# Performance work log

Measured on AMD Instinct MI355X. Metric: run time of the kernel, lower is better.

Reference implementation:

```python
import jax, jax.numpy as jnp
import numpy as np

N = 10000   # nodes
E = 160000  # edges per layer (avg degree 16)
B = 8       # batch of time windows
CIN = 32
S = 32      # spatial_channels
COUT = 32
NEG_SLOPE = 0.01  # F.leaky_relu default


def _xavier(k, shape):
    bound = np.sqrt(6.0 / (shape[0] + shape[1])).astype(np.float32)
    return jax.random.uniform(k, shape, jnp.float32, -bound, bound)


def setup_inputs() -> dict:
    key = jax.random.key(0)
    ks = jax.random.split(key, 20)
    return {
        "X": jax.random.normal(ks[0], (B, N, CIN), jnp.float32),
        "edge_index0": jax.random.randint(ks[1], (2, E), 0, N, jnp.int32),
        "edge_index1": jax.random.randint(ks[2], (2, E), 0, N, jnp.int32),
        "edge_weight0": jax.random.uniform(ks[3], (E,), jnp.float32),
        "edge_weight1": jax.random.uniform(ks[4], (E,), jnp.float32),
        "res_n_id0": jnp.arange(N, dtype=jnp.int32),
        "res_n_id1": jnp.arange(N, dtype=jnp.int32),
        # layer 1 params
        "Wn1": _xavier(ks[5], (CIN, S)),
        "We1": _xavier(ks[6], (1, S)),
        "Q1": _xavier(ks[7], (S, S)),
        "K1": _xavier(ks[8], (S, S)),
        "att_w1": _xavier(ks[9], (3 * S, 1)),
        "att_b1": jnp.zeros((1,), jnp.float32),
        "out_w1": _xavier(ks[10], (2 * S, S)),
        "out_b1": jnp.zeros((S,), jnp.float32),
        # layer 2 params
        "Wn2": _xavier(ks[11], (S, COUT)),
        "We2": _xavier(ks[12], (1, COUT)),
        "Q2": _xavier(ks[13], (COUT, COUT)),
        "K2": _xavier(ks[14], (COUT, COUT)),
        "att_w2": _xavier(ks[15], (3 * COUT, 1)),
        "att_b2": jnp.zeros((1,), jnp.float32),
        "out_w2": _xavier(ks[16], (2 * COUT, COUT)),
        "out_b2": jnp.zeros((COUT,), jnp.float32),
    }


def _egnn_conv(x_src, x_dst, edge_index, edge_w, Wn, We, Q, K, att_w, att_b, out_w, out_b):
    # x_src: [Ns, B, Cin], x_dst: [Nd, B, Cin], edge_index: [2, E], edge_w: [E]
    xs = x_src @ Wn                              # [Ns, B, O]
    xd = x_dst @ Wn                              # [Nd, B, O]
    ee = edge_w[:, None] @ We                    # [E, O]  (edge_channels = 1)
    src, dst = edge_index[0], edge_index[1]
    xj = xs[src]                                 # [E, B, O] gather source feats
    xi = xd[dst]                                 # [E, B, O] gather target feats
    q = xj @ Q                                   # [E, B, O]
    k = xi @ K                                   # [E, B, O]
    eb = jnp.broadcast_to(ee[:, None, :], q.shape)  # [E, B, O]
    att_feature = jnp.concatenate([q, k, eb], axis=-1)          # [E, B, 3O]
    att = jax.nn.sigmoid(att_feature @ att_w + att_b)           # [E, B, 1]
    msg = att * xj * jax.nn.sigmoid(eb)                         # [E, B, O]
    aggr = jnp.zeros_like(xd).at[dst].add(msg)                  # scatter-add -> [Nd, B, O]
    upd = jnp.concatenate([xd, aggr], axis=-1) @ out_w + out_b  # [Nd, B, O]
    return xd + upd


def reference(X, edge_index0, edge_index1, edge_weight0, edge_weight1,
              res_n_id0, res_n_id1,
              Wn1, We1, Q1, K1, att_w1, att_b1, out_w1, out_b1,
              Wn2, We2, Q2, K2, att_w2, att_b2, out_w2, out_b2):
    h = jnp.transpose(X, (1, 0, 2))              # [N, B, CIN]
    h = _egnn_conv(h, h[res_n_id0], edge_index0, edge_weight0,
                   Wn1, We1, Q1, K1, att_w1, att_b1, out_w1, out_b1)
    h = jax.nn.leaky_relu(h, NEG_SLOPE)
    h = _egnn_conv(h, h[res_n_id1], edge_index1, edge_weight1,
                   Wn2, We2, Q2, K2, att_w2, att_b2, out_w2, out_b2)
    h = jax.nn.leaky_relu(h, NEG_SLOPE)
    return jnp.transpose(h, (1, 0, 2))           # [B, N, COUT]
```

## Files before the change

kernel.cpp:

```cpp
#include <hip/hip_runtime.h>

#define NNODES 10000
#define NEDGES 160000
#define NB 8
#define NC 32
#define CAP 96
#define LUTB 2048
#define EBLKS 625
#define LUTBLKS 128
constexpr float NEG_SLOPE = 0.01f;

__device__ __forceinline__ float sigmoidf_(float x) {
    return 1.0f / (1.0f + __expf(-x));
}

__device__ __forceinline__ unsigned pk2bf(float a, float b) {
    unsigned ua = __float_as_uint(a);
    ua = (ua + 0x7fffu + ((ua >> 16) & 1u)) >> 16;
    unsigned ub = __float_as_uint(b);
    ub = (ub + 0x7fffu + ((ub >> 16) & 1u)) & 0xffff0000u;
    return ua | ub;
}

__global__ __launch_bounds__(256) void prologue_kernel(
    const float* Q1, const float* K1, const float* aw1, const float* We1,
    const float* Q2, const float* K2, const float* aw2, const float* We2,
    const int* __restrict__ ei0, const int* __restrict__ ei1,
    const float* __restrict__ ew0, const float* __restrict__ ew1,
    const float* __restrict__ ab1, const float* __restrict__ ab2,
    float* consts, uint2* __restrict__ lut,
    int2* __restrict__ pkw1, int2* __restrict__ pkw2,
    int* __restrict__ cnt,
    unsigned* __restrict__ xs1h, unsigned* __restrict__ xs2h,
    float* __restrict__ sq1, float* __restrict__ sk1,
    const float* __restrict__ X, const float* __restrict__ Wn)
{
    int bx = blockIdx.x;
    int t = threadIdx.x;

    if (bx < 2 * EBLKS) {
        __shared__ float sCE, sAB;
        int layer = bx / EBLKS;
        int e = (bx % EBLKS) * 256 + t;
        const int*   ei = layer ? ei1 : ei0;
        const float* ew = layer ? ew1 : ew0;
        int src = ei[e];
        int dst = ei[NEDGES + e];
        float w = ew[e];
        if (t < 32) {
            const float* We = layer ? We2 : We1;
            const float* aw = layer ? aw2 : aw1;
            float p = We[t] * aw[64 + t];
            #pragma unroll
            for (int m = 16; m >= 1; m >>= 1) p += __shfl_xor(p, m, 32);
            if (t == 0) { sCE = p; sAB = (layer ? ab2 : ab1)[0]; }
        }
        __syncthreads();
        int pos = atomicAdd(&cnt[layer * NNODES + dst], 1);
        if (pos < CAP) {
            int ix = (int)(w * (float)LUTB);
            ix = min(max(ix, 0), LUTB - 1);
            (layer ? pkw2 : pkw1)[(size_t)dst * CAP + pos] =
                make_int2(src | (ix << 14), __float_as_int(w * sCE + sAB));
        }
        return;
    }
    if (bx < 2 * EBLKS + LUTBLKS) {
        int i = (bx - 2 * EBLKS) * 256 + t;
        int layer = i >> 14;
        int bin   = (i >> 3) & (LUTB - 1);
        int o4    = i & 7;
        float w   = (bin + 0.5f) * (1.0f / LUTB);
        const float* We = layer ? We2 : We1;
        float s0 = sigmoidf_(w * We[o4 * 4 + 0]);
        float s1 = sigmoidf_(w * We[o4 * 4 + 1]);
        float s2 = sigmoidf_(w * We[o4 * 4 + 2]);
        float s3 = sigmoidf_(w * We[o4 * 4 + 3]);
        lut[i] = make_uint2(pk2bf(s0, s1), pk2bf(s2, s3));
        if (i < 128) {
            xs1h[(size_t)NNODES * 128 + i] = 0u;
            xs2h[(size_t)NNODES * 128 + i] = 0u;
        }
        return;
    }
    if (bx == 2 * EBLKS + LUTBLKS) {
        if (t < 32) {
            float aq2 = 0.f, ak2 = 0.f;
            for (int s = 0; s < 32; ++s) {
                aq2 += Q2[t * 32 + s] * aw2[s];
                ak2 += K2[t * 32 + s] * aw2[32 + s];
            }
            consts[64 + t] = aq2;
            consts[96 + t] = ak2;
        }
        return;
    }

    __shared__ float wnL[NC * NC];
    __shared__ float aqL[NC], akL[NC];
    __shared__ float xrow[4][NB][NC + 4];
    int w = t >> 6, l = t & 63, b = l >> 3, o4 = l & 7;
    int n = (bx - (2 * EBLKS + LUTBLKS + 1)) * 4 + w;
    for (int i = t; i < NC * NC; i += 256) wnL[i] = Wn[i];
    if (t < 64) {
        int which = t >> 5, o = t & 31;
        const float* M  = which ? K1 : Q1;
        const float* av = aw1 + which * 32;
        float s = 0.f;
        for (int k = 0; k < 32; ++k) s += M[o * 32 + k] * av[k];
        (which ? akL : aqL)[o] = s;
    }
    const float4* X4 = (const float4*)X;
    float4 xv = X4[((size_t)b * NNODES + n) * 8 + o4];
    ((float4*)&xrow[w][b][0])[o4] = xv;
    __syncthreads();
    float4 aq = ((const float4*)aqL)[o4];
    float4 ak = ((const float4*)akL)[o4];
    const float4* wnL4 = (const float4*)wnL;
    float4 acc = {0.f, 0.f, 0.f, 0.f};
    #pragma unroll
    for (int c = 0; c < NC; ++c) {
        float xc = xrow[w][b][c];
        float4 w4 = wnL4[c * 8 + o4];
        acc.x += xc * w4.x; acc.y += xc * w4.y;
        acc.z += xc * w4.z; acc.w += xc * w4.w;
    }
    ((uint2*)xs1h)[(size_t)n * 64 + l] = make_uint2(pk2bf(acc.x, acc.y), pk2bf(acc.z, acc.w));
    float vq = acc.x * aq.x + acc.y * aq.y + acc.z * aq.z + acc.w * aq.w;
    float vk = acc.x * ak.x + acc.y * ak.y + acc.z * ak.z + acc.w * ak.w;
    #pragma unroll
    for (int m = 4; m >= 1; m >>= 1) {
        vq += __shfl_xor(vq, m);
        vk += __shfl_xor(vk, m);
    }
    if (o4 == 0) {
        sq1[n * NB + b] = vq;
        sk1[n * NB + b] = vk;
    }
}

template <int MODE>
__global__ __launch_bounds__(256) void gather_kernel(
    const int* __restrict__ cnt, const int2* __restrict__ pkw,
    const unsigned* __restrict__ xsh,
    const float* __restrict__ sq, const float* __restrict__ sk,
    const uint2* __restrict__ luth,
    const float* __restrict__ consts,
    const float* __restrict__ ow, const float* __restrict__ ob,
    const float* __restrict__ Wn2,
    unsigned* __restrict__ xs2h, float* __restrict__ sq2, float* __restrict__ sk2,
    float* __restrict__ outp)
{
    __shared__ __align__(16) float owL[2 * NC * NC];
    __shared__ __align__(16) float wnL[(MODE == 0) ? NC * NC : 4];
    __shared__ __align__(16) float xL[4][NB][NC];
    __shared__ __align__(16) float aL[4][NB][NC];

    int t = threadIdx.x, w = t >> 6, l = t & 63, b = l >> 3, o4 = l & 7;
    int n = blockIdx.x * 4 + w;
    for (int i = t; i < 2 * NC * NC; i += 256) owL[i] = ow[i];
    if (MODE == 0)
        for (int i = t; i < NC * NC; i += 256) wnL[i] = Wn2[i];
    __syncthreads();

    const float4* owL4 = (const float4*)owL;
    const float4* wnL4 = (const float4*)wnL;
    const uint2*  XH   = (const uint2*)xsh;

    int deg = min(cnt[n], CAP - 24);
    const int2* pp = pkw + (size_t)n * CAP;
    float skb = sk[n * NB + b];

    float4 acc = {0.f, 0.f, 0.f, 0.f};
    int2 mc = pp[o4];
    float sqc = sq[(mc.x & 16383) * NB + b];
    for (int c0 = 0; c0 < deg; c0 += 8) {
        int2 mn = pp[c0 + 8 + o4];
        float sqn = sq[(mn.x & 16383) * NB + b];
        float att_own = (c0 + o4 < deg)
                      ? sigmoidf_(sqc + skb + __int_as_float(mc.y)) : 0.f;
        #pragma unroll
        for (int j = 0; j < 8; ++j) {
            int spk = __builtin_amdgcn_readlane(mc.x, j);
            int ssrc, six;
            if (c0 + j < deg) {
                ssrc = spk & 16383;
                six  = (spk >> 14) & 2047;
            } else {
                ssrc = NNODES;
                six  = 0;
            }
            uint2 hx = XH[(size_t)ssrc * 64 + l];
            uint2 hg = luth[six * 8 + o4];
            float at = __shfl(att_own, b * 8 + j);
            acc.x += at * __uint_as_float(hg.x << 16)          * __uint_as_float(hx.x << 16);
            acc.y += at * __uint_as_float(hg.x & 0xffff0000u)  * __uint_as_float(hx.x & 0xffff0000u);
            acc.z += at * __uint_as_float(hg.y << 16)          * __uint_as_float(hx.y << 16);
            acc.w += at * __uint_as_float(hg.y & 0xffff0000u)  * __uint_as_float(hx.y & 0xffff0000u);
        }
        mc = mn; sqc = sqn;
    }

    uint2 hv = XH[(size_t)n * 64 + l];
    float4 xv;
    xv.x = __uint_as_float(hv.x << 16);
    xv.y = __uint_as_float(hv.x & 0xffff0000u);
    xv.z = __uint_as_float(hv.y << 16);
    xv.w = __uint_as_float(hv.y & 0xffff0000u);
    ((float4*)&xL[w][b][0])[o4] = xv;
    ((float4*)&aL[w][b][0])[o4] = acc;
    float4 u = ((const float4*)ob)[o4];
    #pragma unroll 4
    for (int c = 0; c < NC; ++c) {
        float xc = xL[w][b][c];
        float ac = aL[w][b][c];
        float4 w1 = owL4[c * 8 + o4];
        float4 w2 = owL4[(NC + c) * 8 + o4];
        u.x += xc * w1.x + ac * w2.x;
        u.y += xc * w1.y + ac * w2.y;
        u.z += xc * w1.z + ac * w2.z;
        u.w += xc * w1.w + ac * w2.w;
    }
    float4 r;
    r.x = xv.x + u.x; r.y = xv.y + u.y; r.z = xv.z + u.z; r.w = xv.w + u.w;
    r.x = (r.x > 0.f) ? r.x : NEG_SLOPE * r.x;
    r.y = (r.y > 0.f) ? r.y : NEG_SLOPE * r.y;
    r.z = (r.z > 0.f) ? r.z : NEG_SLOPE * r.z;
    r.w = (r.w > 0.f) ? r.w : NEG_SLOPE * r.w;

    if (MODE == 1) {
        ((float4*)outp)[((size_t)b * NNODES + n) * 8 + o4] = r;
    } else {
        ((float4*)&xL[w][b][0])[o4] = r;
        float4 a2 = {0.f, 0.f, 0.f, 0.f};
        #pragma unroll 4
        for (int c = 0; c < NC; ++c) {
            float hc = xL[w][b][c];
            float4 w0 = wnL4[c * 8 + o4];
            a2.x += hc * w0.x;
            a2.y += hc * w0.y;
            a2.z += hc * w0.z;
            a2.w += hc * w0.w;
        }
        ((uint2*)xs2h)[(size_t)n * 64 + l] = make_uint2(pk2bf(a2.x, a2.y), pk2bf(a2.z, a2.w));
        float4 aqv = ((const float4*)(consts + 64))[o4];
        float4 akv = ((const float4*)(consts + 96))[o4];
        float vq = a2.x*aqv.x + a2.y*aqv.y + a2.z*aqv.z + a2.w*aqv.w;
        float vk = a2.x*akv.x + a2.y*akv.y + a2.z*akv.z + a2.w*akv.w;
        #pragma unroll
        for (int m = 4; m >= 1; m >>= 1) {
            vq += __shfl_xor(vq, m);
            vk += __shfl_xor(vk, m);
        }
        if (o4 == 0) {
            sq2[n * NB + b] = vq;
            sk2[n * NB + b] = vk;
        }
    }
}

extern "C" void kernel_launch(void* const* d_in, const int* in_sizes, int n_in,
                              void* d_out, int out_size, void* d_ws, size_t ws_size,
                              hipStream_t stream) {
    const float* X    = (const float*)d_in[0];
    const int*   ei0  = (const int*)  d_in[1];
    const int*   ei1  = (const int*)  d_in[2];
    const float* ew0  = (const float*)d_in[3];
    const float* ew1  = (const float*)d_in[4];
    const float* Wn1  = (const float*)d_in[7];
    const float* We1  = (const float*)d_in[8];
    const float* Q1   = (const float*)d_in[9];
    const float* K1   = (const float*)d_in[10];
    const float* aw1  = (const float*)d_in[11];
    const float* ab1  = (const float*)d_in[12];
    const float* ow1  = (const float*)d_in[13];
    const float* ob1  = (const float*)d_in[14];
    const float* Wn2  = (const float*)d_in[15];
    const float* We2  = (const float*)d_in[16];
    const float* Q2   = (const float*)d_in[17];
    const float* K2   = (const float*)d_in[18];
    const float* aw2  = (const float*)d_in[19];
    const float* ab2  = (const float*)d_in[20];
    const float* ow2  = (const float*)d_in[21];
    const float* ob2  = (const float*)d_in[22];

    const size_t ROWH = (size_t)(NNODES + 1) * 128;
    const size_t SS   = (size_t)(NNODES + 1) * NB;
    unsigned* XS1H  = (unsigned*)d_ws;
    unsigned* XS2H  = XS1H + ROWH;
    float* SQ1    = (float*)(XS2H + ROWH);
    float* SK1    = SQ1 + SS;
    float* SQ2    = SK1 + SS;
    float* SK2    = SQ2 + SS;
    float* CONSTS = SK2 + SS;
    uint2* LUTH   = (uint2*)(CONSTS + 160);
    int*   CNT    = (int*)(LUTH + 2 * LUTB * 8);
    int2*  PKW1   = (int2*)(CNT + 2 * NNODES);
    int2*  PKW2   = PKW1 + (size_t)NNODES * CAP;

    hipMemsetAsync(CNT, 0, 2 * NNODES * sizeof(int), stream);
    prologue_kernel<<<2 * EBLKS + LUTBLKS + 1 + NNODES / 4, 256, 0, stream>>>(
        Q1, K1, aw1, We1, Q2, K2, aw2, We2, ei0, ei1, ew0, ew1, ab1, ab2,
        CONSTS, LUTH, PKW1, PKW2, CNT, XS1H, XS2H, SQ1, SK1, X, Wn1);

    gather_kernel<0><<<NNODES / 4, 256, 0, stream>>>(
        CNT, PKW1, XS1H, SQ1, SK1, LUTH, CONSTS,
        ow1, ob1, Wn2, XS2H, SQ2, SK2, nullptr);
    gather_kernel<1><<<NNODES / 4, 256, 0, stream>>>(
        CNT + NNODES, PKW2, XS2H, SQ2, SK2, LUTH + LUTB * 8, CONSTS,
        ow2, ob2, nullptr, nullptr, nullptr, nullptr, (float*)d_out);
}
```

Before: 92.81 us.

## Make gather kernels persistent over several nodes and prefetch next node's metadata

Each wave now handles up to three nodes strided by a fixed wave count, with the grid shrunk to match. This amortizes the per-block loading of the output and Wn weights into shared memory. It also prefetches the next node's degree, first packed-edge chunk, sk and sq while the current node is processed. The cost is less parallelism (1000 blocks instead of 2500) and tail imbalance, since some waves get two nodes and others three.

```diff
diff --git a/kernel.cpp b/kernel.cpp
--- a/kernel.cpp
+++ b/kernel.cpp
@@ -8,6 +8,8 @@
 #define LUTB 2048
 #define EBLKS 625
 #define LUTBLKS 128
+#define NWAVES 4000
+#define KNODES 3
 constexpr float NEG_SLOPE = 0.01f;
 
 __device__ __forceinline__ float sigmoidf_(float x) {
@@ -157,7 +159,7 @@
     __shared__ __align__(16) float aL[4][NB][NC];
 
     int t = threadIdx.x, w = t >> 6, l = t & 63, b = l >> 3, o4 = l & 7;
-    int n = blockIdx.x * 4 + w;
+    int wid = blockIdx.x * 4 + w;
     for (int i = t; i < 2 * NC * NC; i += 256) owL[i] = ow[i];
     if (MODE == 0)
         for (int i = t; i < NC * NC; i += 256) wnL[i] = Wn2[i];
@@ -167,95 +169,118 @@
     const float4* wnL4 = (const float4*)wnL;
     const uint2*  XH   = (const uint2*)xsh;
 
-    int deg = min(cnt[n], CAP - 24);
-    const int2* pp = pkw + (size_t)n * CAP;
-    float skb = sk[n * NB + b];
-
-    float4 acc = {0.f, 0.f, 0.f, 0.f};
-    int2 mc = pp[o4];
-    float sqc = sq[(mc.x & 16383) * NB + b];
-    for (int c0 = 0; c0 < deg; c0 += 8) {
-        int2 mn = pp[c0 + 8 + o4];
-        float sqn = sq[(mn.x & 16383) * NB + b];
-        float att_own = (c0 + o4 < deg)
-                      ? sigmoidf_(sqc + skb + __int_as_float(mc.y)) : 0.f;
-        #pragma unroll
-        for (int j = 0; j < 8; ++j) {
-            int spk = __builtin_amdgcn_readlane(mc.x, j);
-            int ssrc, six;
-            if (c0 + j < deg) {
-                ssrc = spk & 16383;
-                six  = (spk >> 14) & 2047;
-            } else {
-                ssrc = NNODES;
-                six  = 0;
-            }
-            uint2 hx = XH[(size_t)ssrc * 64 + l];
-            uint2 hg = luth[six * 8 + o4];
-            float at = __shfl(att_own, b * 8 + j);
-            acc.x += at * __uint_as_float(hg.x << 16)          * __uint_as_float(hx.x << 16);
-            acc.y += at * __uint_as_float(hg.x & 0xffff0000u)  * __uint_as_float(hx.x & 0xffff0000u);
-            acc.z += at * __uint_as_float(hg.y << 16)          * __uint_as_float(hx.y << 16);
-            acc.w += at * __uint_as_float(hg.y & 0xffff0000u)  * __uint_as_float(hx.y & 0xffff0000u);
-        }
-        mc = mn; sqc = sqn;
-    }
-
-    uint2 hv = XH[(size_t)n * 64 + l];
-    float4 xv;
-    xv.x = __uint_as_float(hv.x << 16);
-    xv.y = __uint_as_float(hv.x & 0xffff0000u);
-    xv.z = __uint_as_float(hv.y << 16);
-    xv.w = __uint_as_float(hv.y & 0xffff0000u);
-    ((float4*)&xL[w][b][0])[o4] = xv;
-    ((float4*)&aL[w][b][0])[o4] = acc;
-    float4 u = ((const float4*)ob)[o4];
-    #pragma unroll 4
-    for (int c = 0; c < NC; ++c) {
-        float xc = xL[w][b][c];
-        float ac = aL[w][b][c];
-        float4 w1 = owL4[c * 8 + o4];
-        float4 w2 = owL4[(NC + c) * 8 + o4];
-        u.x += xc * w1.x + ac * w2.x;
-        u.y += xc * w1.y + ac * w2.y;
-        u.z += xc * w1.z + ac * w2.z;
-        u.w += xc * w1.w + ac * w2.w;
-    }
-    float4 r;
-    r.x = xv.x + u.x; r.y = xv.y + u.y; r.z = xv.z + u.z; r.w = xv.w + u.w;
-    r.x = (r.x > 0.f) ? r.x : NEG_SLOPE * r.x;
-    r.y = (r.y > 0.f) ? r.y : NEG_SLOPE * r.y;
-    r.z = (r.z > 0.f) ? r.z : NEG_SLOPE * r.z;
-    r.w = (r.w > 0.f) ? r.w : NEG_SLOPE * r.w;
-
-    if (MODE == 1) {
-        ((float4*)outp)[((size_t)b * NNODES + n) * 8 + o4] = r;
-    } else {
-        ((float4*)&xL[w][b][0])[o4] = r;
-        float4 a2 = {0.f, 0.f, 0.f, 0.f};
+    int degA = cnt[wid];
+    const int2* ppA = pkw + (size_t)wid * CAP;
+    int2  mcA  = ppA[o4];
+    float skbA = sk[wid * NB + b];
+    float sqA  = sq[(mcA.x & 16383) * NB + b];
+
+    for (int k = 0; k < KNODES; ++k) {
+        int n = wid + k * NWAVES;
+        if (n >= NNODES) break;
+        int nn = wid + (k + 1) * NWAVES;
+        bool hasN = (k + 1 < KNODES) && (nn < NNODES);
+
+        int degB = 0; int2 mcB = make_int2((int)NNODES, 0); float skbB = 0.f;
+        const int2* ppB = pkw;
+        if (hasN) {
+            degB = cnt[nn];
+            ppB  = pkw + (size_t)nn * CAP;
+            mcB  = ppB[o4];
+            skbB = sk[nn * NB + b];
+        }
+
+        int deg = min(degA, CAP - 24);
+        float4 acc = {0.f, 0.f, 0.f, 0.f};
+        int2 mc = mcA; float sqc = sqA;
+        for (int c0 = 0; c0 < deg; c0 += 8) {
+            int2 mn = ppA[c0 + 8 + o4];
+            float sqn = sq[(mn.x & 16383) * NB + b];
+            float att_own = (c0 + o4 < deg)
+                          ? sigmoidf_(sqc + skbA + __int_as_float(mc.y)) : 0.f;
+            #pragma unroll
+            for (int j = 0; j < 8; ++j) {
+                int spk = __builtin_amdgcn_readlane(mc.x, j);
+                int ssrc, six;
+                if (c0 + j < deg) {
+                    ssrc = spk & 16383;
+                    six  = (spk >> 14) & 2047;
+                } else {
+                    ssrc = NNODES;
+                    six  = 0;
+                }
+                uint2 hx = XH[(size_t)ssrc * 64 + l];
+                uint2 hg = luth[six * 8 + o4];
+                float at = __shfl(att_own, b * 8 + j);
+                acc.x += at * __uint_as_float(hg.x << 16)          * __uint_as_float(hx.x << 16);
+                acc.y += at * __uint_as_float(hg.x & 0xffff0000u)  * __uint_as_float(hx.x & 0xffff0000u);
+                acc.z += at * __uint_as_float(hg.y << 16)          * __uint_as_float(hx.y << 16);
+                acc.w += at * __uint_as_float(hg.y & 0xffff0000u)  * __uint_as_float(hx.y & 0xffff0000u);
+            }
+            mc = mn; sqc = sqn;
+        }
+
+        float sqB = 0.f;
+        if (hasN) sqB = sq[(mcB.x & 16383) * NB + b];
+
+        uint2 hv = XH[(size_t)n * 64 + l];
+        float4 xv;
+        xv.x = __uint_as_float(hv.x << 16);
+        xv.y = __uint_as_float(hv.x & 0xffff0000u);
+        xv.z = __uint_as_float(hv.y << 16);
+        xv.w = __uint_as_float(hv.y & 0xffff0000u);
+        ((float4*)&xL[w][b][0])[o4] = xv;
+        ((float4*)&aL[w][b][0])[o4] = acc;
+        float4 u = ((const float4*)ob)[o4];
         #pragma unroll 4
         for (int c = 0; c < NC; ++c) {
-            float hc = xL[w][b][c];
-            float4 w0 = wnL4[c * 8 + o4];
-            a2.x += hc * w0.x;
-            a2.y += hc * w0.y;
-            a2.z += hc * w0.z;
-            a2.w += hc * w0.w;
-        }
-        ((uint2*)xs2h)[(size_t)n * 64 + l] = make_uint2(pk2bf(a2.x, a2.y), pk2bf(a2.z, a2.w));
-        float4 aqv = ((const float4*)(consts + 64))[o4];
-        float4 akv = ((const float4*)(consts + 96))[o4];
-        float vq = a2.x*aqv.x + a2.y*aqv.y + a2.z*aqv.z + a2.w*aqv.w;
-        float vk = a2.x*akv.x + a2.y*akv.y + a2.z*akv.z + a2.w*akv.w;
-        #pragma unroll
-        for (int m = 4; m >= 1; m >>= 1) {
-            vq += __shfl_xor(vq, m);
-            vk += __shfl_xor(vk, m);
-        }
-        if (o4 == 0) {
-            sq2[n * NB + b] = vq;
-            sk2[n * NB + b] = vk;
-        }
+            float xc = xL[w][b][c];
+            float ac = aL[w][b][c];
+            float4 w1 = owL4[c * 8 + o4];
+            float4 w2 = owL4[(NC + c) * 8 + o4];
+            u.x += xc * w1.x + ac * w2.x;
+            u.y += xc * w1.y + ac * w2.y;
+            u.z += xc * w1.z + ac * w2.z;
+            u.w += xc * w1.w + ac * w2.w;
+        }
+        float4 r;
+        r.x = xv.x + u.x; r.y = xv.y + u.y; r.z = xv.z + u.z; r.w = xv.w + u.w;
+        r.x = (r.x > 0.f) ? r.x : NEG_SLOPE * r.x;
+        r.y = (r.y > 0.f) ? r.y : NEG_SLOPE * r.y;
+        r.z = (r.z > 0.f) ? r.z : NEG_SLOPE * r.z;
+        r.w = (r.w > 0.f) ? r.w : NEG_SLOPE * r.w;
+
+        if (MODE == 1) {
+            ((float4*)outp)[((size_t)b * NNODES + n) * 8 + o4] = r;
+        } else {
+            ((float4*)&xL[w][b][0])[o4] = r;
+            float4 a2 = {0.f, 0.f, 0.f, 0.f};
+            #pragma unroll 4
+            for (int c = 0; c < NC; ++c) {
+                float hc = xL[w][b][c];
+                float4 w0 = wnL4[c * 8 + o4];
+                a2.x += hc * w0.x;
+                a2.y += hc * w0.y;
+                a2.z += hc * w0.z;
+                a2.w += hc * w0.w;
+            }
+            ((uint2*)xs2h)[(size_t)n * 64 + l] = make_uint2(pk2bf(a2.x, a2.y), pk2bf(a2.z, a2.w));
+            float4 aqv = ((const float4*)(consts + 64))[o4];
+            float4 akv = ((const float4*)(consts + 96))[o4];
+            float vq = a2.x*aqv.x + a2.y*aqv.y + a2.z*aqv.z + a2.w*aqv.w;
+            float vk = a2.x*akv.x + a2.y*akv.y + a2.z*akv.z + a2.w*akv.w;
+            #pragma unroll
+            for (int m = 4; m >= 1; m >>= 1) {
+                vq += __shfl_xor(vq, m);
+                vk += __shfl_xor(vk, m);
+            }
+            if (o4 == 0) {
+                sq2[n * NB + b] = vq;
+                sk2[n * NB + b] = vk;
+            }
+        }
+
+        degA = degB; ppA = ppB; mcA = mcB; skbA = skbB; sqA = sqB;
     }
 }
 
@@ -303,10 +328,10 @@
         Q1, K1, aw1, We1, Q2, K2, aw2, We2, ei0, ei1, ew0, ew1, ab1, ab2,
         CONSTS, LUTH, PKW1, PKW2, CNT, XS1H, XS2H, SQ1, SK1, X, Wn1);
 
-    gather_kernel<0><<<NNODES / 4, 256, 0, stream>>>(
+    gather_kernel<0><<<NWAVES / 4, 256, 0, stream>>>(
         CNT, PKW1, XS1H, SQ1, SK1, LUTH, CONSTS,
         ow1, ob1, Wn2, XS2H, SQ2, SK2, nullptr);
-    gather_kernel<1><<<NNODES / 4, 256, 0, stream>>>(
+    gather_kernel<1><<<NWAVES / 4, 256, 0, stream>>>(
         CNT + NNODES, PKW2, XS2H, SQ2, SK2, LUTH + LUTB * 8, CONSTS,
         ow2, ob2, nullptr, nullptr, nullptr, nullptr, (float*)d_out);
 }
```

Result: faster. 88.81 us (-4.3%).
